# Optimization experiments

Measured on AMD Instinct MI355X. Metric: run time of the kernel, lower is better.

Reference implementation:

```python
import jax, jax.numpy as jnp
import numpy as np

B, T, C, H, W = 1, 7, 128, 64, 64
IC = C // 2
MB = 256  # codebook size (hardcoded in source)


def setup_inputs() -> dict:
    key = jax.random.key(0)
    ks = jax.random.split(key, 15)
    rn = lambda k, s, sc=1.0: sc * jax.random.normal(k, s, dtype=jnp.float32)
    return {
        "x": rn(ks[0], (B, T, C, H, W)),
        "gn_gamma": 1.0 + rn(ks[1], (C,), 0.1),
        "gn_beta": rn(ks[2], (C,), 0.1),
        "g_w": rn(ks[3], (IC, C), 0.05), "g_b": rn(ks[4], (IC,), 0.05),
        "theta_w": rn(ks[5], (IC, C), 0.05), "theta_b": rn(ks[6], (IC,), 0.05),
        "phi_w": rn(ks[7], (IC, C), 0.05), "phi_b": rn(ks[8], (IC,), 0.05),
        "wz_w": rn(ks[9], (C, IC * 7), 0.05), "wz_b": rn(ks[10], (C,), 0.05),
        "wz1_w": rn(ks[11], (C, IC), 0.05), "wz1_b": rn(ks[12], (C,), 0.05),
        "mb": rn(ks[13], (IC, MB)),
        "std": 4.0 * jnp.ones((1,), jnp.float32),
    }


def _groupnorm(v, gamma, beta, groups=32, eps=1e-6):
    # v: (B_, C_, H_, W_)
    b_ = v.shape[0]
    vr = v.reshape(b_, groups, -1)
    mu = vr.mean(axis=-1, keepdims=True)
    var = vr.var(axis=-1, keepdims=True)
    vn = ((vr - mu) * jax.lax.rsqrt(var + eps)).reshape(v.shape)
    return vn * gamma[:, None, None] + beta[:, None, None]


def _conv1x1(v, w, b):
    # v: (B_, Cin, H, W), w: (Cout, Cin)
    return jnp.einsum('bchw,oc->bohw', v, w) + b[:, None, None]


def reference(x, gn_gamma, gn_beta, g_w, g_b, theta_w, theta_b, phi_w, phi_b,
              wz_w, wz_b, wz1_w, wz1_b, mb, std):
    b, t, c, h, w = x.shape
    ic = g_w.shape[0]
    n = h * w

    # distance matrix D[(i,j),(k,l)] = (j-l)^2 + (i-k)^2  (row-major flatten of (i,j))
    yy, xx = jnp.meshgrid(jnp.arange(h), jnp.arange(w), indexing='ij')
    yf = yy.reshape(-1).astype(x.dtype)
    xf = xx.reshape(-1).astype(x.dtype)
    D = (xf[:, None] - xf[None, :]) ** 2 + (yf[:, None] - yf[None, :]) ** 2  # (n, n)
    weight = jnp.exp(-0.5 * D / (std[0] * std[0]))  # (n, n)

    q = x[:, 3]  # (b, c, h, w)
    hn = _groupnorm(x.reshape(b * t, c, h, w), gn_gamma, gn_beta)
    qn = _groupnorm(q, gn_gamma, gn_beta)

    g_x = _conv1x1(hn, g_w, g_b).reshape(b, t, ic, n)
    theta_x = _conv1x1(hn, theta_w, theta_b).reshape(b, t, ic, n)
    phi = _conv1x1(qn, phi_w, phi_b).reshape(b, ic, n).transpose(0, 2, 1)  # (b, n, ic)

    def frame(_, tg):
        theta_t, g_t = tg  # each (b, ic, n)
        f = jnp.einsum('bnc,bcm->bnm', phi, theta_t)        # (b, n, n)
        fdc = jax.nn.softmax(f, axis=-1) * weight            # post-softmax reweight
        y = jnp.einsum('bnm,bcm->bnc', fdc, g_t)            # (b, n, ic)
        return None, y

    _, ys = jax.lax.scan(frame, None,
                         (theta_x.transpose(1, 0, 2, 3), g_x.transpose(1, 0, 2, 3)))
    # ys: (t, b, n, ic) -> (b, t*ic, h, w)
    corr = ys.transpose(1, 0, 3, 2).reshape(b, t * ic, h, w)
    W_y = _conv1x1(corr, wz_w, wz_b)

    # codebook memory attention
    f1 = jnp.einsum('bnc,ck->bnk', phi, mb) * (float(ic) ** -0.5)
    fdc1 = jax.nn.softmax(f1, axis=-1)
    y1 = jnp.einsum('bnk,ck->bnc', fdc1, mb)  # (b, n, ic)
    qloss = jnp.mean(jnp.abs(phi - y1))
    y1 = y1.transpose(0, 2, 1).reshape(b, ic, h, w)
    W_y1 = _conv1x1(y1, wz1_w, wz1_b)

    z = W_y + q + W_y1
    return z, qloss
```

## Files before the change

### kernel.cpp

```cpp
#include <hip/hip_runtime.h>
#include <hip/hip_bf16.h>

#define TT 7
#define CCH 128
#define ICH 64
#define NHW 4096
#define NSPLIT 2
#define MCHUNK (NHW/NSPLIT)
#define NSEFF (NSPLIT*4)

typedef __attribute__((ext_vector_type(8))) short short8;
typedef __attribute__((ext_vector_type(4))) short sshort4;
typedef __attribute__((ext_vector_type(4))) float floatx4;

#define LOG2E 1.44269504f

#if defined(__has_builtin)
#if __has_builtin(__builtin_amdgcn_mfma_f32_16x16x16bf16_1k)
#define MFMA16(A,B,C) __builtin_amdgcn_mfma_f32_16x16x16bf16_1k(A,B,C,0,0,0)
#elif __has_builtin(__builtin_amdgcn_mfma_f32_16x16x16_bf16)
#define MFMA16(A,B,C) __builtin_amdgcn_mfma_f32_16x16x16_bf16(A,B,C,0,0,0)
#endif
#endif
#ifndef MFMA16
#define MFMA16(A,B,C) __builtin_amdgcn_mfma_f32_16x16x16bf16_1k(A,B,C,0,0,0)
#endif

static __device__ __forceinline__ short f2bf(float f){
  __hip_bfloat16 h = __float2bfloat16(f);
  return *reinterpret_cast<short*>(&h);
}
static __device__ __forceinline__ float bf2f(short s){
  __hip_bfloat16 h = *reinterpret_cast<__hip_bfloat16*>(&s);
  return __bfloat162float(h);
}

__global__ __launch_bounds__(256) void k_stats(const float* __restrict__ x,
                                               float* __restrict__ sacc,
                                               float* __restrict__ s2acc){
  int b = blockIdx.x;
  int t = b >> 7, c = b & 127;
  const float4* base = reinterpret_cast<const float4*>(x + ((size_t)t*CCH + c)*NHW);
  float s = 0.f, s2 = 0.f;
  #pragma unroll
  for (int k = 0; k < 4; ++k){
    float4 v = base[k*256 + threadIdx.x];
    s  += v.x + v.y + v.z + v.w;
    s2 += v.x*v.x + v.y*v.y + v.z*v.z + v.w*v.w;
  }
  #pragma unroll
  for (int off = 32; off; off >>= 1){
    s  += __shfl_xor(s, off);
    s2 += __shfl_xor(s2, off);
  }
  __shared__ float sh[8];
  int w = threadIdx.x >> 6;
  if ((threadIdx.x & 63) == 0){ sh[w] = s; sh[4+w] = s2; }
  __syncthreads();
  if (threadIdx.x == 0){
    atomicAdd(&sacc [t*32 + (c>>2)], sh[0]+sh[1]+sh[2]+sh[3]);
    atomicAdd(&s2acc[t*32 + (c>>2)], sh[4]+sh[5]+sh[6]+sh[7]);
  }
}

__global__ __launch_bounds__(256) void k_cast(const float* __restrict__ x,
                                              __hip_bfloat16* __restrict__ xbf){
  __shared__ short tile[64][66];
  int t = blockIdx.y, n0 = blockIdx.x*64, zh = blockIdx.z;
  int ln = threadIdx.x & 63, cq = threadIdx.x >> 6;
  #pragma unroll 4
  for (int ci = 0; ci < 16; ++ci){
    int cl = cq*16 + ci;
    tile[ln][cl] = f2bf(x[((size_t)t*CCH + zh*64 + cl)*NHW + n0 + ln]);
  }
  __syncthreads();
  int row = threadIdx.x >> 2, seg = threadIdx.x & 3;
  short* dst = reinterpret_cast<short*>(xbf) + ((size_t)t*NHW + n0 + row)*CCH + zh*64 + seg*16;
  #pragma unroll
  for (int k = 0; k < 2; ++k){
    short8 v;
    #pragma unroll
    for (int j = 0; j < 8; ++j) v[j] = tile[row][seg*16 + k*8 + j];
    *reinterpret_cast<short8*>(dst + k*8) = v;
  }
}

__global__ void k_setup(const float* __restrict__ gw, const float* __restrict__ gb,
                        const float* __restrict__ thw, const float* __restrict__ thb,
                        const float* __restrict__ phw, const float* __restrict__ phb,
                        const float* __restrict__ gamma, const float* __restrict__ beta,
                        const float* __restrict__ sacc, const float* __restrict__ s2acc,
                        __hip_bfloat16* __restrict__ Wth, float* __restrict__ bth,
                        __hip_bfloat16* __restrict__ Wg,  float* __restrict__ bg,
                        __hip_bfloat16* __restrict__ Wphi, float* __restrict__ bphi,
                        const float* __restrict__ wz, const float* __restrict__ wz1,
                        const float* __restrict__ wz_b, const float* __restrict__ wz1_b,
                        const float* __restrict__ mb,
                        __hip_bfloat16* __restrict__ wzcat, float* __restrict__ biasz,
                        __hip_bfloat16* __restrict__ mbT, __hip_bfloat16* __restrict__ mbbf){
  if (blockIdx.x < 4){
    int idx = blockIdx.x*256 + threadIdx.x;
    if (idx >= 960) return;
    const float *W, *B; __hip_bfloat16 *Wf; float *bfo; int t, o;
    if (idx < 448){ t = idx >> 6; o = idx & 63; W = thw; B = thb; Wf = Wth + ((size_t)t*ICH + o)*CCH; bfo = bth + t*64 + o; }
    else if (idx < 896){ int j = idx - 448; t = j >> 6; o = j & 63; W = gw; B = gb; Wf = Wg + ((size_t)t*ICH + o)*CCH; bfo = bg + t*64 + o; }
    else { t = 3; o = idx - 896; W = phw; B = phb; Wf = Wphi + (size_t)o*CCH; bfo = bphi + o; }
    float bias = B[o];
    for (int c = 0; c < CCH; ++c){
      int g = c >> 2;
      float m  = sacc [t*32+g] * (1.f/16384.f);
      float vr = s2acc[t*32+g] * (1.f/16384.f) - m*m;
      float rs = rsqrtf(vr + 1e-6f);
      float a = gamma[c]*rs;
      float w = W[o*CCH + c];
      Wf[c] = __float2bfloat16(w * a);
      bias += w * (beta[c] - m*a);
    }
    *bfo = bias;
  } else {
    int idx = (blockIdx.x - 4)*256 + threadIdx.x;
    if (idx < 128*512){
      int o = idx >> 9, k = idx & 511;
      float v = (k < 448) ? wz[o*448 + k] : wz1[o*64 + (k-448)];
      wzcat[idx] = __float2bfloat16(v);
    }
    if (idx < 128) biasz[idx] = wz_b[idx] + wz1_b[idx];
    if (idx < 64*256){
      int c = idx >> 8, j = idx & 255;
      float v = mb[idx];
      mbbf[idx] = __float2bfloat16(v);
      mbT[j*64 + c] = __float2bfloat16(v);
    }
  }
}

__global__ __launch_bounds__(256) void k_conv(const __hip_bfloat16* __restrict__ xbf,
    const __hip_bfloat16* __restrict__ Wth, const float* __restrict__ bth,
    const __hip_bfloat16* __restrict__ Wg,  const float* __restrict__ bg,
    const __hip_bfloat16* __restrict__ Wphi, const float* __restrict__ bphi,
    __hip_bfloat16* __restrict__ thetaT, __hip_bfloat16* __restrict__ g_nat,
    __hip_bfloat16* __restrict__ phi_bf){
  const int t = blockIdx.y, n0 = blockIdx.x*64;
  const int w = threadIdx.x >> 6, lane = threadIdx.x & 63;
  const int l15 = lane & 15, quad = lane >> 4;

  const short* xb = reinterpret_cast<const short*>(xbf) + ((size_t)t*NHW + n0)*CCH;
  short8 B[4][4];
  #pragma unroll
  for (int nt = 0; nt < 4; ++nt)
    #pragma unroll
    for (int kk = 0; kk < 4; ++kk)
      B[nt][kk] = *reinterpret_cast<const short8*>(xb + (size_t)(nt*16 + l15)*CCH + kk*32 + quad*8);

  {
    const short* aw = reinterpret_cast<const short*>(Wth) + ((size_t)t*ICH + w*16 + l15)*CCH + quad*8;
    short8 A[4];
    #pragma unroll
    for (int kk = 0; kk < 4; ++kk) A[kk] = *reinterpret_cast<const short8*>(aw + kk*32);
    float4 bv = *reinterpret_cast<const float4*>(bth + t*64 + w*16 + quad*4);
    #pragma unroll
    for (int nt = 0; nt < 4; ++nt){
      floatx4 acc = (floatx4){0.f,0.f,0.f,0.f};
      #pragma unroll
      for (int kk = 0; kk < 4; ++kk) acc = __builtin_amdgcn_mfma_f32_16x16x32_bf16(A[kk], B[nt][kk], acc, 0, 0, 0);
      sshort4 pk;
      pk[0] = f2bf(acc[0] + bv.x); pk[1] = f2bf(acc[1] + bv.y);
      pk[2] = f2bf(acc[2] + bv.z); pk[3] = f2bf(acc[3] + bv.w);
      short* dst = reinterpret_cast<short*>(thetaT) + ((size_t)t*NHW + n0 + nt*16 + l15)*ICH + w*16 + quad*4;
      *reinterpret_cast<sshort4*>(dst) = pk;
    }
  }
  {
    const short* aw = reinterpret_cast<const short*>(Wg) + ((size_t)t*ICH + w*16 + l15)*CCH + quad*8;
    short8 A[4];
    #pragma unroll
    for (int kk = 0; kk < 4; ++kk) A[kk] = *reinterpret_cast<const short8*>(aw + kk*32);
    float4 bv = *reinterpret_cast<const float4*>(bg + t*64 + w*16 + quad*4);
    #pragma unroll
    for (int nt = 0; nt < 4; ++nt){
      floatx4 acc = (floatx4){0.f,0.f,0.f,0.f};
      #pragma unroll
      for (int kk = 0; kk < 4; ++kk) acc = __builtin_amdgcn_mfma_f32_16x16x32_bf16(A[kk], B[nt][kk], acc, 0, 0, 0);
      short* gb = reinterpret_cast<short*>(g_nat);
      float bvv[4] = {bv.x, bv.y, bv.z, bv.w};
      #pragma unroll
      for (int r = 0; r < 4; ++r)
        gb[((size_t)t*ICH + w*16 + quad*4 + r)*NHW + n0 + nt*16 + l15] = f2bf(acc[r] + bvv[r]);
    }
  }
  if (t == 3){
    const short* aw = reinterpret_cast<const short*>(Wphi) + (size_t)(w*16 + l15)*CCH + quad*8;
    short8 A[4];
    #pragma unroll
    for (int kk = 0; kk < 4; ++kk) A[kk] = *reinterpret_cast<const short8*>(aw + kk*32);
    float4 bv = *reinterpret_cast<const float4*>(bphi + w*16 + quad*4);
    #pragma unroll
    for (int nt = 0; nt < 4; ++nt){
      floatx4 acc = (floatx4){0.f,0.f,0.f,0.f};
      #pragma unroll
      for (int kk = 0; kk < 4; ++kk) acc = __builtin_amdgcn_mfma_f32_16x16x32_bf16(A[kk], B[nt][kk], acc, 0, 0, 0);
      sshort4 pk;
      pk[0] = f2bf(acc[0] + bv.x); pk[1] = f2bf(acc[1] + bv.y);
      pk[2] = f2bf(acc[2] + bv.z); pk[3] = f2bf(acc[3] + bv.w);
      short* dst = reinterpret_cast<short*>(phi_bf) + (size_t)(n0 + nt*16 + l15)*ICH + w*16 + quad*4;
      *reinterpret_cast<sshort4*>(dst) = pk;
    }
  }
}

__global__ __launch_bounds__(256, 3) void k_attn(
    const __hip_bfloat16* __restrict__ phi_bf,
    const __hip_bfloat16* __restrict__ thetaT,
    const __hip_bfloat16* __restrict__ g_nat,
    const float* __restrict__ stdp,
    float* __restrict__ Opart, float* __restrict__ Zpart)
{
  const int t    = blockIdx.z;
  const int sp   = blockIdx.y;
  const int w    = threadIdx.x >> 6;
  const int lane = threadIdx.x & 63;
  const int l15  = lane & 15;
  const int quad = lane >> 4;
  const int n0   = blockIdx.x*64;
  const int yn   = blockIdx.x;

  const float sstd  = stdp[0];
  const float coefL = -0.5f / (sstd*sstd) * LOG2E;

  const short* phi_s = reinterpret_cast<const short*>(phi_bf);
  const short* th_s  = reinterpret_cast<const short*>(thetaT) + (size_t)t*NHW*ICH;
  const short* g_s   = reinterpret_cast<const short*>(g_nat)  + (size_t)t*ICH*NHW;

  short8 phB[4][2];
  #pragma unroll
  for (int nt = 0; nt < 4; ++nt){
    const short* pp = phi_s + (size_t)(n0 + nt*16 + l15)*ICH + quad*8;
    phB[nt][0] = *reinterpret_cast<const short8*>(pp);
    phB[nt][1] = *reinterpret_cast<const short8*>(pp + 32);
  }

  float wxv[4][4];
  {
    const int xm = w*16 + quad*4;
    #pragma unroll
    for (int nt = 0; nt < 4; ++nt){
      int xn = nt*16 + l15;
      #pragma unroll
      for (int r = 0; r < 4; ++r){
        int dx = xn - (xm + r);
        wxv[nt][r] = exp2f(coefL * (float)(dx*dx));
      }
    }
  }

  floatx4 oacc[4][4];
  #pragma unroll
  for (int a = 0; a < 4; ++a)
    #pragma unroll
    for (int b = 0; b < 4; ++b) oacc[a][b] = (floatx4){0.f,0.f,0.f,0.f};
  float psum[4] = {0.f,0.f,0.f,0.f};

  const int mbeg = sp*MCHUNK;
  const short* thp = th_s + (size_t)(mbeg + w*16 + l15)*ICH + quad*8;
  const short* gp0 = g_s + (size_t)( 0 + l15)*NHW + mbeg + w*16 + quad*4;
  const short* gp1 = g_s + (size_t)(16 + l15)*NHW + mbeg + w*16 + quad*4;
  const short* gp2 = g_s + (size_t)(32 + l15)*NHW + mbeg + w*16 + quad*4;
  const short* gp3 = g_s + (size_t)(48 + l15)*NHW + mbeg + w*16 + quad*4;

  const int ymb = mbeg >> 6;
  for (int it = 0; it < MCHUNK/64; ++it){
    short8 a0 = *reinterpret_cast<const short8*>(thp);
    short8 a1 = *reinterpret_cast<const short8*>(thp + 32);
    thp += 64*ICH;
    sshort4 ga0 = *reinterpret_cast<const sshort4*>(gp0); gp0 += 64;
    sshort4 ga1 = *reinterpret_cast<const sshort4*>(gp1); gp1 += 64;
    sshort4 ga2 = *reinterpret_cast<const sshort4*>(gp2); gp2 += 64;
    sshort4 ga3 = *reinterpret_cast<const sshort4*>(gp3); gp3 += 64;

    floatx4 s[4];
    #pragma unroll
    for (int nt = 0; nt < 4; ++nt){
      floatx4 acc = (floatx4){0.f,0.f,0.f,0.f};
      acc = __builtin_amdgcn_mfma_f32_16x16x32_bf16(a0, phB[nt][0], acc, 0, 0, 0);
      s[nt] = __builtin_amdgcn_mfma_f32_16x16x32_bf16(a1, phB[nt][1], acc, 0, 0, 0);
    }

    const int dy = yn - (ymb + it);
    const float wyv = exp2f(coefL * (float)(dy*dy));
    sshort4 pB[4];
    #pragma unroll
    for (int nt = 0; nt < 4; ++nt){
      #pragma unroll
      for (int r = 0; r < 4; ++r){
        float p = exp2f(s[nt][r] * LOG2E);
        psum[nt] += p;
        pB[nt][r] = f2bf(p * (wyv * wxv[nt][r]));
      }
    }

    #pragma unroll
    for (int nt = 0; nt < 4; ++nt){
      oacc[0][nt] = MFMA16(ga0, pB[nt], oacc[0][nt]);
      oacc[1][nt] = MFMA16(ga1, pB[nt], oacc[1][nt]);
      oacc[2][nt] = MFMA16(ga2, pB[nt], oacc[2][nt]);
      oacc[3][nt] = MFMA16(ga3, pB[nt], oacc[3][nt]);
    }
  }

  const int si = t*NSEFF + sp*4 + w;
  float* Ob = Opart + (size_t)si*ICH*NHW;
  #pragma unroll
  for (int ct = 0; ct < 4; ++ct)
    #pragma unroll
    for (int nt = 0; nt < 4; ++nt){
      int c = ct*16 + quad*4;
      int n = n0 + nt*16 + l15;
      #pragma unroll
      for (int r = 0; r < 4; ++r)
        Ob[(size_t)(c + r)*NHW + n] = oacc[ct][nt][r];
    }
  #pragma unroll
  for (int nt = 0; nt < 4; ++nt){
    float z = psum[nt];
    z += __shfl_xor(z, 16);
    z += __shfl_xor(z, 32);
    psum[nt] = z;
  }
  if (quad == 0){
    #pragma unroll
    for (int nt = 0; nt < 4; ++nt)
      Zpart[(size_t)si*NHW + n0 + nt*16 + l15] = psum[nt];
  }
}

__global__ __launch_bounds__(256) void k_merge(const float* __restrict__ Opart,
    const float* __restrict__ Zpart, __hip_bfloat16* __restrict__ corrT){
  __shared__ short tile[64][72];
  __shared__ float zinv[64];
  const int t = blockIdx.y, n0 = blockIdx.x*64;

  if (threadIdx.x < 64){
    float zs = 0.f;
    #pragma unroll
    for (int s = 0; s < NSEFF; ++s)
      zs += Zpart[(size_t)(t*NSEFF + s)*NHW + n0 + threadIdx.x];
    zinv[threadIdx.x] = 1.f / zs;
  }
  __syncthreads();

  const int nq = threadIdx.x & 15, cc = threadIdx.x >> 4;
  #pragma unroll
  for (int cp = 0; cp < 4; ++cp){
    int c = cp*16 + cc;
    float4 acc = {0.f,0.f,0.f,0.f};
    #pragma unroll
    for (int s = 0; s < NSEFF; ++s){
      float4 v = *reinterpret_cast<const float4*>(
        Opart + ((size_t)(t*NSEFF + s)*ICH + c)*NHW + n0 + nq*4);
      acc.x += v.x; acc.y += v.y; acc.z += v.z; acc.w += v.w;
    }
    tile[nq*4+0][c] = f2bf(acc.x * zinv[nq*4+0]);
    tile[nq*4+1][c] = f2bf(acc.y * zinv[nq*4+1]);
    tile[nq*4+2][c] = f2bf(acc.z * zinv[nq*4+2]);
    tile[nq*4+3][c] = f2bf(acc.w * zinv[nq*4+3]);
  }
  __syncthreads();

  #pragma unroll
  for (int rep = 0; rep < 2; ++rep){
    int idx = rep*256 + threadIdx.x;
    int n = idx >> 3, seg = idx & 7;
    short8 v = *reinterpret_cast<short8*>(&tile[n][seg*8]);
    *reinterpret_cast<short8*>(reinterpret_cast<short*>(corrT)
        + (size_t)(n0 + n)*512 + t*64 + seg*8) = v;
  }
}

__global__ __launch_bounds__(256) void k_mb(const __hip_bfloat16* __restrict__ phi_bf,
    const __hip_bfloat16* __restrict__ mbT, const __hip_bfloat16* __restrict__ mbbf,
    __hip_bfloat16* __restrict__ corrT, float* __restrict__ qacc){
  const int n0 = blockIdx.x*32;
  const int w = threadIdx.x >> 6, lane = threadIdx.x & 63;
  const int l15 = lane & 15, quad = lane >> 4;

  __shared__ short P[32][264];
  __shared__ float Zsh[4][32];

  const short* phi_s = reinterpret_cast<const short*>(phi_bf);
  const short* mbT_s = reinterpret_cast<const short*>(mbT);
  const short* mb_s  = reinterpret_cast<const short*>(mbbf);

  short8 Bp[2][2];
  #pragma unroll
  for (int nt = 0; nt < 2; ++nt){
    const short* pp = phi_s + (size_t)(n0 + nt*16 + l15)*ICH + quad*8;
    Bp[nt][0] = *reinterpret_cast<const short8*>(pp);
    Bp[nt][1] = *reinterpret_cast<const short8*>(pp + 32);
  }
  float psum[2] = {0.f, 0.f};
  #pragma unroll
  for (int jt = 0; jt < 4; ++jt){
    const short* ap = mbT_s + (size_t)(w*64 + jt*16 + l15)*64 + quad*8;
    short8 A0 = *reinterpret_cast<const short8*>(ap);
    short8 A1 = *reinterpret_cast<const short8*>(ap + 32);
    #pragma unroll
    for (int nt = 0; nt < 2; ++nt){
      floatx4 acc = (floatx4){0.f,0.f,0.f,0.f};
      acc = __builtin_amdgcn_mfma_f32_16x16x32_bf16(A0, Bp[nt][0], acc, 0, 0, 0);
      acc = __builtin_amdgcn_mfma_f32_16x16x32_bf16(A1, Bp[nt][1], acc, 0, 0, 0);
      sshort4 pk;
      #pragma unroll
      for (int r = 0; r < 4; ++r){
        float p = exp2f(acc[r] * (0.125f*LOG2E));
        psum[nt] += p;
        pk[r] = f2bf(p);
      }
      *reinterpret_cast<sshort4*>(&P[nt*16 + l15][w*64 + jt*16 + quad*4]) = pk;
    }
  }
  #pragma unroll
  for (int nt = 0; nt < 2; ++nt){
    float z = psum[nt];
    z += __shfl_xor(z, 16);
    z += __shfl_xor(z, 32);
    if (quad == 0) Zsh[w][nt*16 + l15] = z;
  }
  __syncthreads();

  float ql = 0.f;
  #pragma unroll
  for (int nt = 0; nt < 2; ++nt){
    floatx4 acc = (floatx4){0.f,0.f,0.f,0.f};
    #pragma unroll
    for (int kk = 0; kk < 8; ++kk){
      const short* ap = mb_s + (size_t)(w*16 + l15)*256 + kk*32 + quad*8;
      short8 A = *reinterpret_cast<const short8*>(ap);
      short8 B = *reinterpret_cast<const short8*>(&P[nt*16 + l15][kk*32 + quad*8]);
      acc = __builtin_amdgcn_mfma_f32_16x16x32_bf16(A, B, acc, 0, 0, 0);
    }
    int nn = nt*16 + l15;
    float zt = Zsh[0][nn] + Zsh[1][nn] + Zsh[2][nn] + Zsh[3][nn];
    float rz = 1.f / zt;
    const short* ph = phi_s + (size_t)(n0 + nn)*ICH + w*16 + quad*4;
    sshort4 ph4 = *reinterpret_cast<const sshort4*>(ph);
    sshort4 pk;
    #pragma unroll
    for (int r = 0; r < 4; ++r){
      float y = acc[r] * rz;
      ql += fabsf(bf2f(ph4[r]) - y);
      pk[r] = f2bf(y);
    }
    short* dst = reinterpret_cast<short*>(corrT) + (size_t)(n0 + nn)*512 + 448 + w*16 + quad*4;
    *reinterpret_cast<sshort4*>(dst) = pk;
  }
  #pragma unroll
  for (int off = 32; off; off >>= 1) ql += __shfl_xor(ql, off);
  if (lane == 0) atomicAdd(qacc, ql);
}

__global__ __launch_bounds__(256) void k_z(const __hip_bfloat16* __restrict__ corrT,
    const __hip_bfloat16* __restrict__ wzcat, const float* __restrict__ biasz,
    const float* __restrict__ x, const float* __restrict__ qacc,
    float* __restrict__ out){
  const int n0 = blockIdx.x*16;
  const int w = threadIdx.x >> 6, lane = threadIdx.x & 63;
  const int l15 = lane & 15, quad = lane >> 4;
  const int o0 = blockIdx.y*64 + w*16;

  const short* ct_s = reinterpret_cast<const short*>(corrT) + (size_t)(n0 + l15)*512 + quad*8;
  const short* wz_s = reinterpret_cast<const short*>(wzcat) + (size_t)(o0 + l15)*512 + quad*8;

  floatx4 acc = (floatx4){0.f,0.f,0.f,0.f};
  #pragma unroll
  for (int kk = 0; kk < 16; ++kk){
    short8 A = *reinterpret_cast<const short8*>(wz_s + kk*32);
    short8 B = *reinterpret_cast<const short8*>(ct_s + kk*32);
    acc = __builtin_amdgcn_mfma_f32_16x16x32_bf16(A, B, acc, 0, 0, 0);
  }
  float4 bz = *reinterpret_cast<const float4*>(biasz + o0 + quad*4);
  float bzv[4] = {bz.x, bz.y, bz.z, bz.w};
  #pragma unroll
  for (int r = 0; r < 4; ++r){
    int o = o0 + quad*4 + r;
    int n = n0 + l15;
    float q = x[((size_t)3*CCH + o)*NHW + n];
    out[(size_t)o*NHW + n] = acc[r] + bzv[r] + q;
  }
  if (blockIdx.x == 0 && blockIdx.y == 0 && threadIdx.x == 0)
    out[(size_t)CCH*NHW] = qacc[0] * (1.f/262144.f);
}

extern "C" void kernel_launch(void* const* d_in, const int* in_sizes, int n_in,
                              void* d_out, int out_size, void* d_ws, size_t ws_size,
                              hipStream_t stream){
  const float* x     = (const float*)d_in[0];
  const float* gamma = (const float*)d_in[1];
  const float* beta  = (const float*)d_in[2];
  const float* g_w   = (const float*)d_in[3];
  const float* g_b   = (const float*)d_in[4];
  const float* th_w  = (const float*)d_in[5];
  const float* th_b  = (const float*)d_in[6];
  const float* ph_w  = (const float*)d_in[7];
  const float* ph_b  = (const float*)d_in[8];
  const float* wz_w  = (const float*)d_in[9];
  const float* wz_b  = (const float*)d_in[10];
  const float* wz1_w = (const float*)d_in[11];
  const float* wz1_b = (const float*)d_in[12];
  const float* mb    = (const float*)d_in[13];
  const float* stdp  = (const float*)d_in[14];
  float* out = (float*)d_out;

  char* ws = (char*)d_ws;
  size_t off = 0;
  auto alloc = [&](size_t bytes)->char*{
    char* p = ws + off; off += (bytes + 255) & ~(size_t)255; return p;
  };
  float* zbuf    = (float*)alloc(452*4);
  float* sacc    = zbuf;
  float* s2acc   = zbuf + 224;
  float* qacc    = zbuf + 448;
  __hip_bfloat16* xbf    = (__hip_bfloat16*)alloc((size_t)TT*NHW*CCH*2);
  __hip_bfloat16* Wth    = (__hip_bfloat16*)alloc((size_t)TT*ICH*CCH*2);
  float* bth             = (float*)alloc(TT*64*4);
  __hip_bfloat16* Wg     = (__hip_bfloat16*)alloc((size_t)TT*ICH*CCH*2);
  float* bg              = (float*)alloc(TT*64*4);
  __hip_bfloat16* Wphi   = (__hip_bfloat16*)alloc((size_t)ICH*CCH*2);
  float* bphi            = (float*)alloc(64*4);
  __hip_bfloat16* wzcat  = (__hip_bfloat16*)alloc((size_t)128*512*2);
  float* biasz           = (float*)alloc(128*4);
  __hip_bfloat16* mbT    = (__hip_bfloat16*)alloc((size_t)256*64*2);
  __hip_bfloat16* mbbf   = (__hip_bfloat16*)alloc((size_t)64*256*2);
  __hip_bfloat16* thetaT = (__hip_bfloat16*)alloc((size_t)TT*NHW*ICH*2);
  __hip_bfloat16* g_nat  = (__hip_bfloat16*)alloc((size_t)TT*NHW*ICH*2);
  __hip_bfloat16* phi_bf = (__hip_bfloat16*)alloc((size_t)NHW*ICH*2);
  __hip_bfloat16* corrT  = (__hip_bfloat16*)alloc((size_t)NHW*512*2);
  float* Opart   = (float*)alloc((size_t)TT*NSEFF*ICH*NHW*4);
  float* Zpart   = (float*)alloc((size_t)TT*NSEFF*NHW*4);

  hipMemsetAsync(zbuf, 0, 452*4, stream);
  k_stats<<<896, 256, 0, stream>>>(x, sacc, s2acc);
  k_cast <<<dim3(64,7,2), 256, 0, stream>>>(x, xbf);
  k_setup<<<260, 256, 0, stream>>>(g_w, g_b, th_w, th_b, ph_w, ph_b, gamma, beta,
                                   sacc, s2acc, Wth, bth, Wg, bg, Wphi, bphi,
                                   wz_w, wz1_w, wz_b, wz1_b, mb, wzcat, biasz, mbT, mbbf);
  k_conv <<<dim3(64,7), 256, 0, stream>>>(xbf, Wth, bth, Wg, bg, Wphi, bphi,
                                          thetaT, g_nat, phi_bf);
  k_attn <<<dim3(64,NSPLIT,7), 256, 0, stream>>>(phi_bf, thetaT, g_nat, stdp, Opart, Zpart);
  k_merge<<<dim3(64,7), 256, 0, stream>>>(Opart, Zpart, corrT);
  k_mb   <<<128, 256, 0, stream>>>(phi_bf, mbT, mbbf, corrT, qacc);
  k_z    <<<dim3(256,2), 256, 0, stream>>>(corrT, wzcat, biasz, x, qacc, out);
}
```

Measured before the change: 267.4 us.

## Fuse stats into cast, merge attention partials in-block, parallelize setup

Group-norm statistics are now computed inside the bf16 cast kernel, so x is read once instead of twice. The attention kernel drops the split over the key dimension: each block handles 32 queries over all 4096 keys and reduces its four waves' partial outputs through shared memory. It then writes the normalized bf16 result directly, which removes the large fp32 Opart/Zpart buffers and the separate merge kernel. The weight-folding setup is spread across 240 blocks with one wave per output row and a shuffle reduction. The cost is fewer warps of parallelism per query and extra shared memory in the attention kernel.

```diff
diff --git a/kernel.cpp b/kernel.cpp
--- a/kernel.cpp
+++ b/kernel.cpp
@@ -5,9 +5,6 @@
 #define CCH 128
 #define ICH 64
 #define NHW 4096
-#define NSPLIT 2
-#define MCHUNK (NHW/NSPLIT)
-#define NSEFF (NSPLIT*4)
 
 typedef __attribute__((ext_vector_type(8))) short short8;
 typedef __attribute__((ext_vector_type(4))) short sshort4;
@@ -35,43 +32,34 @@
   return __bfloat162float(h);
 }
 
-__global__ __launch_bounds__(256) void k_stats(const float* __restrict__ x,
-                                               float* __restrict__ sacc,
-                                               float* __restrict__ s2acc){
-  int b = blockIdx.x;
-  int t = b >> 7, c = b & 127;
-  const float4* base = reinterpret_cast<const float4*>(x + ((size_t)t*CCH + c)*NHW);
-  float s = 0.f, s2 = 0.f;
-  #pragma unroll
-  for (int k = 0; k < 4; ++k){
-    float4 v = base[k*256 + threadIdx.x];
-    s  += v.x + v.y + v.z + v.w;
-    s2 += v.x*v.x + v.y*v.y + v.z*v.z + v.w*v.w;
-  }
-  #pragma unroll
-  for (int off = 32; off; off >>= 1){
-    s  += __shfl_xor(s, off);
-    s2 += __shfl_xor(s2, off);
-  }
-  __shared__ float sh[8];
-  int w = threadIdx.x >> 6;
-  if ((threadIdx.x & 63) == 0){ sh[w] = s; sh[4+w] = s2; }
-  __syncthreads();
-  if (threadIdx.x == 0){
-    atomicAdd(&sacc [t*32 + (c>>2)], sh[0]+sh[1]+sh[2]+sh[3]);
-    atomicAdd(&s2acc[t*32 + (c>>2)], sh[4]+sh[5]+sh[6]+sh[7]);
-  }
-}
-
-__global__ __launch_bounds__(256) void k_cast(const float* __restrict__ x,
-                                              __hip_bfloat16* __restrict__ xbf){
+__global__ __launch_bounds__(256) void k_precast(const float* __restrict__ x,
+    __hip_bfloat16* __restrict__ xbf, float* __restrict__ sacc, float* __restrict__ s2acc){
   __shared__ short tile[64][66];
   int t = blockIdx.y, n0 = blockIdx.x*64, zh = blockIdx.z;
-  int ln = threadIdx.x & 63, cq = threadIdx.x >> 6;
+  int ln = threadIdx.x & 63, w = threadIdx.x >> 6;
+  float sl[4] = {0.f,0.f,0.f,0.f}, s2l[4] = {0.f,0.f,0.f,0.f};
   #pragma unroll 4
   for (int ci = 0; ci < 16; ++ci){
-    int cl = cq*16 + ci;
-    tile[ln][cl] = f2bf(x[((size_t)t*CCH + zh*64 + cl)*NHW + n0 + ln]);
+    int cl = w*16 + ci;
+    float v = x[((size_t)t*CCH + zh*64 + cl)*NHW + n0 + ln];
+    tile[ln][cl] = f2bf(v);
+    sl[ci>>2]  += v;
+    s2l[ci>>2] += v*v;
+  }
+  #pragma unroll
+  for (int off = 32; off; off >>= 1){
+    #pragma unroll
+    for (int g = 0; g < 4; ++g){
+      sl[g]  += __shfl_xor(sl[g],  off);
+      s2l[g] += __shfl_xor(s2l[g], off);
+    }
+  }
+  if (ln == 0){
+    #pragma unroll
+    for (int g = 0; g < 4; ++g){
+      atomicAdd(&sacc [t*32 + zh*16 + w*4 + g], sl[g]);
+      atomicAdd(&s2acc[t*32 + zh*16 + w*4 + g], s2l[g]);
+    }
   }
   __syncthreads();
   int row = threadIdx.x >> 2, seg = threadIdx.x & 3;
@@ -85,44 +73,51 @@
   }
 }
 
-__global__ void k_setup(const float* __restrict__ gw, const float* __restrict__ gb,
-                        const float* __restrict__ thw, const float* __restrict__ thb,
-                        const float* __restrict__ phw, const float* __restrict__ phb,
-                        const float* __restrict__ gamma, const float* __restrict__ beta,
-                        const float* __restrict__ sacc, const float* __restrict__ s2acc,
-                        __hip_bfloat16* __restrict__ Wth, float* __restrict__ bth,
-                        __hip_bfloat16* __restrict__ Wg,  float* __restrict__ bg,
-                        __hip_bfloat16* __restrict__ Wphi, float* __restrict__ bphi,
-                        const float* __restrict__ wz, const float* __restrict__ wz1,
-                        const float* __restrict__ wz_b, const float* __restrict__ wz1_b,
-                        const float* __restrict__ mb,
-                        __hip_bfloat16* __restrict__ wzcat, float* __restrict__ biasz,
-                        __hip_bfloat16* __restrict__ mbT, __hip_bfloat16* __restrict__ mbbf){
-  if (blockIdx.x < 4){
-    int idx = blockIdx.x*256 + threadIdx.x;
-    if (idx >= 960) return;
+__global__ __launch_bounds__(256) void k_setup(
+    const float* __restrict__ gw, const float* __restrict__ gb,
+    const float* __restrict__ thw, const float* __restrict__ thb,
+    const float* __restrict__ phw, const float* __restrict__ phb,
+    const float* __restrict__ gamma, const float* __restrict__ beta,
+    const float* __restrict__ sacc, const float* __restrict__ s2acc,
+    __hip_bfloat16* __restrict__ Wth, float* __restrict__ bth,
+    __hip_bfloat16* __restrict__ Wg,  float* __restrict__ bg,
+    __hip_bfloat16* __restrict__ Wphi, float* __restrict__ bphi,
+    const float* __restrict__ wz, const float* __restrict__ wz1,
+    const float* __restrict__ wz_b, const float* __restrict__ wz1_b,
+    const float* __restrict__ mb,
+    __hip_bfloat16* __restrict__ wzcat, float* __restrict__ biasz,
+    __hip_bfloat16* __restrict__ mbT, __hip_bfloat16* __restrict__ mbbf){
+  if (blockIdx.x < 240){
+    int w = threadIdx.x >> 6, lane = threadIdx.x & 63;
+    int oidx = blockIdx.x*4 + w;
     const float *W, *B; __hip_bfloat16 *Wf; float *bfo; int t, o;
-    if (idx < 448){ t = idx >> 6; o = idx & 63; W = thw; B = thb; Wf = Wth + ((size_t)t*ICH + o)*CCH; bfo = bth + t*64 + o; }
-    else if (idx < 896){ int j = idx - 448; t = j >> 6; o = j & 63; W = gw; B = gb; Wf = Wg + ((size_t)t*ICH + o)*CCH; bfo = bg + t*64 + o; }
-    else { t = 3; o = idx - 896; W = phw; B = phb; Wf = Wphi + (size_t)o*CCH; bfo = bphi + o; }
-    float bias = B[o];
-    for (int c = 0; c < CCH; ++c){
+    if (oidx < 448){ t = oidx >> 6; o = oidx & 63; W = thw; B = thb; Wf = Wth + ((size_t)t*ICH + o)*CCH; bfo = bth + t*64 + o; }
+    else if (oidx < 896){ int j = oidx - 448; t = j >> 6; o = j & 63; W = gw; B = gb; Wf = Wg + ((size_t)t*ICH + o)*CCH; bfo = bg + t*64 + o; }
+    else { t = 3; o = oidx - 896; W = phw; B = phb; Wf = Wphi + (size_t)o*CCH; bfo = bphi + o; }
+    float bp = 0.f;
+    #pragma unroll
+    for (int h = 0; h < 2; ++h){
+      int c = h*64 + lane;
       int g = c >> 2;
       float m  = sacc [t*32+g] * (1.f/16384.f);
       float vr = s2acc[t*32+g] * (1.f/16384.f) - m*m;
       float rs = rsqrtf(vr + 1e-6f);
-      float a = gamma[c]*rs;
-      float w = W[o*CCH + c];
-      Wf[c] = __float2bfloat16(w * a);
-      bias += w * (beta[c] - m*a);
-    }
-    *bfo = bias;
+      float a  = gamma[c]*rs;
+      float wv = W[o*CCH + c];
+      Wf[c] = __float2bfloat16(wv * a);
+      bp += wv * (beta[c] - m*a);
+    }
+    #pragma unroll
+    for (int off = 32; off; off >>= 1) bp += __shfl_xor(bp, off);
+    if (lane == 0) *bfo = bp + B[o];
   } else {
-    int idx = (blockIdx.x - 4)*256 + threadIdx.x;
-    if (idx < 128*512){
-      int o = idx >> 9, k = idx & 511;
-      float v = (k < 448) ? wz[o*448 + k] : wz1[o*64 + (k-448)];
-      wzcat[idx] = __float2bfloat16(v);
+    int idx = (blockIdx.x - 240)*256 + threadIdx.x;
+    #pragma unroll
+    for (int k = 0; k < 2; ++k){
+      int i = idx + k*32768;
+      int o = i >> 9, kk = i & 511;
+      float v = (kk < 448) ? wz[o*448 + kk] : wz1[o*64 + (kk-448)];
+      wzcat[i] = __float2bfloat16(v);
     }
     if (idx < 128) biasz[idx] = wz_b[idx] + wz1_b[idx];
     if (idx < 64*256){
@@ -208,21 +203,24 @@
   }
 }
 
-__global__ __launch_bounds__(256, 3) void k_attn(
+__global__ __launch_bounds__(256, 4) void k_attn(
     const __hip_bfloat16* __restrict__ phi_bf,
     const __hip_bfloat16* __restrict__ thetaT,
     const __hip_bfloat16* __restrict__ g_nat,
     const float* __restrict__ stdp,
-    float* __restrict__ Opart, float* __restrict__ Zpart)
+    __hip_bfloat16* __restrict__ corrT)
 {
-  const int t    = blockIdx.z;
-  const int sp   = blockIdx.y;
+  const int t    = blockIdx.y;
   const int w    = threadIdx.x >> 6;
   const int lane = threadIdx.x & 63;
   const int l15  = lane & 15;
   const int quad = lane >> 4;
-  const int n0   = blockIdx.x*64;
-  const int yn   = blockIdx.x;
+  const int n0   = blockIdx.x*32;
+  const int yn   = n0 >> 6;
+  const int xb0  = n0 & 63;
+
+  __shared__ float Ored[4][32][68];
+  __shared__ float Zsh[4][32];
 
   const float sstd  = stdp[0];
   const float coefL = -0.5f / (sstd*sstd) * LOG2E;
@@ -231,20 +229,20 @@
   const short* th_s  = reinterpret_cast<const short*>(thetaT) + (size_t)t*NHW*ICH;
   const short* g_s   = reinterpret_cast<const short*>(g_nat)  + (size_t)t*ICH*NHW;
 
-  short8 phB[4][2];
-  #pragma unroll
-  for (int nt = 0; nt < 4; ++nt){
+  short8 phB[2][2];
+  #pragma unroll
+  for (int nt = 0; nt < 2; ++nt){
     const short* pp = phi_s + (size_t)(n0 + nt*16 + l15)*ICH + quad*8;
     phB[nt][0] = *reinterpret_cast<const short8*>(pp);
     phB[nt][1] = *reinterpret_cast<const short8*>(pp + 32);
   }
 
-  float wxv[4][4];
+  float wxv[2][4];
   {
     const int xm = w*16 + quad*4;
     #pragma unroll
-    for (int nt = 0; nt < 4; ++nt){
-      int xn = nt*16 + l15;
+    for (int nt = 0; nt < 2; ++nt){
+      int xn = xb0 + nt*16 + l15;
       #pragma unroll
       for (int r = 0; r < 4; ++r){
         int dx = xn - (xm + r);
@@ -253,22 +251,20 @@
     }
   }
 
-  floatx4 oacc[4][4];
+  floatx4 oacc[4][2];
   #pragma unroll
   for (int a = 0; a < 4; ++a)
     #pragma unroll
-    for (int b = 0; b < 4; ++b) oacc[a][b] = (floatx4){0.f,0.f,0.f,0.f};
-  float psum[4] = {0.f,0.f,0.f,0.f};
-
-  const int mbeg = sp*MCHUNK;
-  const short* thp = th_s + (size_t)(mbeg + w*16 + l15)*ICH + quad*8;
-  const short* gp0 = g_s + (size_t)( 0 + l15)*NHW + mbeg + w*16 + quad*4;
-  const short* gp1 = g_s + (size_t)(16 + l15)*NHW + mbeg + w*16 + quad*4;
-  const short* gp2 = g_s + (size_t)(32 + l15)*NHW + mbeg + w*16 + quad*4;
-  const short* gp3 = g_s + (size_t)(48 + l15)*NHW + mbeg + w*16 + quad*4;
-
-  const int ymb = mbeg >> 6;
-  for (int it = 0; it < MCHUNK/64; ++it){
+    for (int b = 0; b < 2; ++b) oacc[a][b] = (floatx4){0.f,0.f,0.f,0.f};
+  float psum[2] = {0.f, 0.f};
+
+  const short* thp = th_s + (size_t)(w*16 + l15)*ICH + quad*8;
+  const short* gp0 = g_s + (size_t)( 0 + l15)*NHW + w*16 + quad*4;
+  const short* gp1 = g_s + (size_t)(16 + l15)*NHW + w*16 + quad*4;
+  const short* gp2 = g_s + (size_t)(32 + l15)*NHW + w*16 + quad*4;
+  const short* gp3 = g_s + (size_t)(48 + l15)*NHW + w*16 + quad*4;
+
+  for (int it = 0; it < 64; ++it){
     short8 a0 = *reinterpret_cast<const short8*>(thp);
     short8 a1 = *reinterpret_cast<const short8*>(thp + 32);
     thp += 64*ICH;
@@ -277,19 +273,19 @@
     sshort4 ga2 = *reinterpret_cast<const sshort4*>(gp2); gp2 += 64;
     sshort4 ga3 = *reinterpret_cast<const sshort4*>(gp3); gp3 += 64;
 
-    floatx4 s[4];
-    #pragma unroll
-    for (int nt = 0; nt < 4; ++nt){
+    floatx4 s[2];
+    #pragma unroll
+    for (int nt = 0; nt < 2; ++nt){
       floatx4 acc = (floatx4){0.f,0.f,0.f,0.f};
       acc = __builtin_amdgcn_mfma_f32_16x16x32_bf16(a0, phB[nt][0], acc, 0, 0, 0);
       s[nt] = __builtin_amdgcn_mfma_f32_16x16x32_bf16(a1, phB[nt][1], acc, 0, 0, 0);
     }
 
-    const int dy = yn - (ymb + it);
+    const int dy = yn - it;
     const float wyv = exp2f(coefL * (float)(dy*dy));
-    sshort4 pB[4];
-    #pragma unroll
-    for (int nt = 0; nt < 4; ++nt){
+    sshort4 pB[2];
+    #pragma unroll
+    for (int nt = 0; nt < 2; ++nt){
       #pragma unroll
       for (int r = 0; r < 4; ++r){
         float p = exp2f(s[nt][r] * LOG2E);
@@ -299,7 +295,7 @@
     }
 
     #pragma unroll
-    for (int nt = 0; nt < 4; ++nt){
+    for (int nt = 0; nt < 2; ++nt){
       oacc[0][nt] = MFMA16(ga0, pB[nt], oacc[0][nt]);
       oacc[1][nt] = MFMA16(ga1, pB[nt], oacc[1][nt]);
       oacc[2][nt] = MFMA16(ga2, pB[nt], oacc[2][nt]);
@@ -307,72 +303,37 @@
     }
   }
 
-  const int si = t*NSEFF + sp*4 + w;
-  float* Ob = Opart + (size_t)si*ICH*NHW;
   #pragma unroll
   for (int ct = 0; ct < 4; ++ct)
     #pragma unroll
-    for (int nt = 0; nt < 4; ++nt){
-      int c = ct*16 + quad*4;
-      int n = n0 + nt*16 + l15;
-      #pragma unroll
-      for (int r = 0; r < 4; ++r)
-        Ob[(size_t)(c + r)*NHW + n] = oacc[ct][nt][r];
-    }
-  #pragma unroll
-  for (int nt = 0; nt < 4; ++nt){
+    for (int nt = 0; nt < 2; ++nt){
+      float4 v;
+      v.x = oacc[ct][nt][0]; v.y = oacc[ct][nt][1];
+      v.z = oacc[ct][nt][2]; v.w = oacc[ct][nt][3];
+      *reinterpret_cast<float4*>(&Ored[w][nt*16 + l15][ct*16 + quad*4]) = v;
+    }
+  #pragma unroll
+  for (int nt = 0; nt < 2; ++nt){
     float z = psum[nt];
     z += __shfl_xor(z, 16);
     z += __shfl_xor(z, 32);
-    psum[nt] = z;
-  }
-  if (quad == 0){
-    #pragma unroll
-    for (int nt = 0; nt < 4; ++nt)
-      Zpart[(size_t)si*NHW + n0 + nt*16 + l15] = psum[nt];
-  }
-}
-
-__global__ __launch_bounds__(256) void k_merge(const float* __restrict__ Opart,
-    const float* __restrict__ Zpart, __hip_bfloat16* __restrict__ corrT){
-  __shared__ short tile[64][72];
-  __shared__ float zinv[64];
-  const int t = blockIdx.y, n0 = blockIdx.x*64;
-
-  if (threadIdx.x < 64){
-    float zs = 0.f;
-    #pragma unroll
-    for (int s = 0; s < NSEFF; ++s)
-      zs += Zpart[(size_t)(t*NSEFF + s)*NHW + n0 + threadIdx.x];
-    zinv[threadIdx.x] = 1.f / zs;
+    if (quad == 0) Zsh[w][nt*16 + l15] = z;
   }
   __syncthreads();
 
-  const int nq = threadIdx.x & 15, cc = threadIdx.x >> 4;
-  #pragma unroll
-  for (int cp = 0; cp < 4; ++cp){
-    int c = cp*16 + cc;
-    float4 acc = {0.f,0.f,0.f,0.f};
-    #pragma unroll
-    for (int s = 0; s < NSEFF; ++s){
-      float4 v = *reinterpret_cast<const float4*>(
-        Opart + ((size_t)(t*NSEFF + s)*ICH + c)*NHW + n0 + nq*4);
-      acc.x += v.x; acc.y += v.y; acc.z += v.z; acc.w += v.w;
-    }
-    tile[nq*4+0][c] = f2bf(acc.x * zinv[nq*4+0]);
-    tile[nq*4+1][c] = f2bf(acc.y * zinv[nq*4+1]);
-    tile[nq*4+2][c] = f2bf(acc.z * zinv[nq*4+2]);
-    tile[nq*4+3][c] = f2bf(acc.w * zinv[nq*4+3]);
-  }
-  __syncthreads();
-
-  #pragma unroll
-  for (int rep = 0; rep < 2; ++rep){
-    int idx = rep*256 + threadIdx.x;
-    int n = idx >> 3, seg = idx & 7;
-    short8 v = *reinterpret_cast<short8*>(&tile[n][seg*8]);
+  {
+    int n = threadIdx.x >> 3, c8 = threadIdx.x & 7;
+    float zt = Zsh[0][n] + Zsh[1][n] + Zsh[2][n] + Zsh[3][n];
+    float rz = 1.f / zt;
+    short8 pk;
+    #pragma unroll
+    for (int j = 0; j < 8; ++j){
+      float o = Ored[0][n][c8*8+j] + Ored[1][n][c8*8+j]
+              + Ored[2][n][c8*8+j] + Ored[3][n][c8*8+j];
+      pk[j] = f2bf(o * rz);
+    }
     *reinterpret_cast<short8*>(reinterpret_cast<short*>(corrT)
-        + (size_t)(n0 + n)*512 + t*64 + seg*8) = v;
+        + (size_t)(n0 + n)*512 + t*64 + c8*8) = pk;
   }
 }
 
@@ -534,19 +495,15 @@
   __hip_bfloat16* g_nat  = (__hip_bfloat16*)alloc((size_t)TT*NHW*ICH*2);
   __hip_bfloat16* phi_bf = (__hip_bfloat16*)alloc((size_t)NHW*ICH*2);
   __hip_bfloat16* corrT  = (__hip_bfloat16*)alloc((size_t)NHW*512*2);
-  float* Opart   = (float*)alloc((size_t)TT*NSEFF*ICH*NHW*4);
-  float* Zpart   = (float*)alloc((size_t)TT*NSEFF*NHW*4);
 
   hipMemsetAsync(zbuf, 0, 452*4, stream);
-  k_stats<<<896, 256, 0, stream>>>(x, sacc, s2acc);
-  k_cast <<<dim3(64,7,2), 256, 0, stream>>>(x, xbf);
-  k_setup<<<260, 256, 0, stream>>>(g_w, g_b, th_w, th_b, ph_w, ph_b, gamma, beta,
+  k_precast<<<dim3(64,7,2), 256, 0, stream>>>(x, xbf, sacc, s2acc);
+  k_setup<<<368, 256, 0, stream>>>(g_w, g_b, th_w, th_b, ph_w, ph_b, gamma, beta,
                                    sacc, s2acc, Wth, bth, Wg, bg, Wphi, bphi,
                                    wz_w, wz1_w, wz_b, wz1_b, mb, wzcat, biasz, mbT, mbbf);
-  k_conv <<<dim3(64,7), 256, 0, stream>>>(xbf, Wth, bth, Wg, bg, Wphi, bphi,
-                                          thetaT, g_nat, phi_bf);
-  k_attn <<<dim3(64,NSPLIT,7), 256, 0, stream>>>(phi_bf, thetaT, g_nat, stdp, Opart, Zpart);
-  k_merge<<<dim3(64,7), 256, 0, stream>>>(Opart, Zpart, corrT);
-  k_mb   <<<128, 256, 0, stream>>>(phi_bf, mbT, mbbf, corrT, qacc);
-  k_z    <<<dim3(256,2), 256, 0, stream>>>(corrT, wzcat, biasz, x, qacc, out);
-}
+  k_conv<<<dim3(64,7), 256, 0, stream>>>(xbf, Wth, bth, Wg, bg, Wphi, bphi,
+                                         thetaT, g_nat, phi_bf);
+  k_attn<<<dim3(128,7), 256, 0, stream>>>(phi_bf, thetaT, g_nat, stdp, corrT);
+  k_mb  <<<128, 256, 0, stream>>>(phi_bf, mbT, mbbf, corrT, qacc);
+  k_z   <<<dim3(256,2), 256, 0, stream>>>(corrT, wzcat, biasz, x, qacc, out);
+}
```

New measurement: 325.6 us. 1.22x slower.
